# Kernel tuning notes

Measured on AMD Instinct MI355X. Metric: run time of the kernel, lower is better.

The kernel has to match this reference:

```python
import jax, jax.numpy as jnp
import numpy as np

H = 4      # num_heads
DH = 32    # head dim (hidden_size // num_heads)


def _seg_softmax(logits, seg, n):
    # numerically stable segment softmax over axis 0, segments of size n
    m = jax.ops.segment_max(logits, seg, num_segments=n)
    e = jnp.exp(logits - m[seg])
    s = jax.ops.segment_sum(e, seg, num_segments=n)
    return e / (s[seg] + 1e-16)


def setup_inputs() -> dict:
    key = jax.random.key(0)
    ks = jax.random.split(key, 16)
    N, E, EE, C = 50000, 400000, 800000, 800000
    NIN, EIN, HID, EMB = 1, 32, 128, 32
    inp = {
        'x': jax.random.normal(ks[0], (N, NIN), jnp.float32),
        'edge_index': jax.random.randint(ks[1], (2, E), 0, N),
        'edge_attr': jax.random.normal(ks[2], (E, EIN), jnp.float32),
        'edge_to_edge_index': jax.random.randint(ks[3], (2, EE), 0, E),
        'node_to_node_index': jax.random.randint(ks[4], (2, C), 0, N),
        'W1': jax.random.normal(ks[5], (2 * NIN + EIN, EMB), jnp.float32) / np.sqrt(2 * NIN + EIN),
        'b1': jnp.zeros((EMB,), jnp.float32),
        'W2': jax.random.normal(ks[6], (EMB, HID), jnp.float32) / np.sqrt(EMB),
        'b2': jnp.zeros((HID,), jnp.float32),
        'Wq': jax.random.normal(ks[7], (HID, HID), jnp.float32) / np.sqrt(HID),
        'Wk': jax.random.normal(ks[8], (HID, HID), jnp.float32) / np.sqrt(HID),
        'Wv': jax.random.normal(ks[9], (HID, HID), jnp.float32) / np.sqrt(HID),
        'Wq2': jax.random.normal(ks[10], (1, HID), jnp.float32),
        'Wk2': jax.random.normal(ks[11], (1, HID), jnp.float32),
        'Wv2': jax.random.normal(ks[12], (1, HID), jnp.float32),
    }
    return inp


def reference(x, edge_index, edge_attr, edge_to_edge_index, node_to_node_index,
              W1, b1, W2, b2, Wq, Wk, Wv, Wq2, Wk2, Wv2):
    N = x.shape[0]
    E = edge_attr.shape[0]
    # --- NodeToEdgeAggregation: gather endpoint node feats, concat edge attr, MLP ---
    s, d = edge_index[0], edge_index[1]
    h = jnp.concatenate([x[s], x[d], edge_attr], axis=-1)          # [E, 2*nin+ein]
    h = jax.nn.relu(h @ W1 + b1) @ W2 + b2                          # [E, hidden]
    # --- EdgeToEdgeAggregation: multi-head attention on the line graph ---
    es, ed = edge_to_edge_index[0], edge_to_edge_index[1]
    q = (h @ Wq)[ed].reshape(-1, H, DH)                             # [EE, H, DH]
    k = (h @ Wk)[es].reshape(-1, H, DH)
    v = (h @ Wv)[es].reshape(-1, H, DH)
    logits = (q * k).sum(-1) / jnp.sqrt(jnp.float32(DH))            # [EE, H]
    alpha = _seg_softmax(logits, ed, E)                             # softmax over incoming edge-neighbors
    agg_e = jax.ops.segment_sum(alpha[..., None] * v, ed, num_segments=E)  # [E, H, DH]
    updated_edge_feat = agg_e.reshape(E, -1).mean(axis=1, keepdims=True)   # [E, 1]
    # --- EdgeToNodeAggregation over combined node+edge feature array ---
    nef = jnp.concatenate([x, updated_edge_feat], axis=0)           # [N+E, 1]
    ns, nd = node_to_node_index[0], node_to_node_index[1]
    q2 = (nef[nd] @ Wq2).reshape(-1, H, DH)                         # [C, H, DH]
    k2 = (nef[ns] @ Wk2).reshape(-1, H, DH)
    v2 = (nef[ns] @ Wv2).reshape(-1, H, DH)
    logits2 = (q2 * k2).sum(-1) / jnp.sqrt(jnp.float32(DH))         # [C, H]
    alpha2 = _seg_softmax(logits2, nd, N + E)
    msgs = (alpha2[..., None] * v2).reshape(ns.shape[0], -1).mean(axis=1)  # [C]
    aggregated_node_feat = jax.ops.segment_sum(msgs, nd, num_segments=N)   # [N]
    return (aggregated_node_feat, updated_edge_feat)
```

## Files before the change

kernel.cpp:

```cpp
#include <hip/hip_runtime.h>
#include <stdint.h>

#define HIDN 128
#define EMBN 32
#define PCAP 16
#define NCAP 64
#define PSEGSH 10
#define NSEGSH 7
#define PSEG (1 << PSEGSH)
#define NSEG (1 << NSEGSH)
#define PBCAP 2816
#define NBCAP 2816
#define CHUNK 2048
#define MAXBINS 400

typedef __attribute__((ext_vector_type(8))) short bf16x8;
typedef __attribute__((ext_vector_type(4))) float f32x4;
typedef unsigned long long u64;

__device__ __forceinline__ unsigned bf16r(float f) {
  unsigned u = __float_as_uint(f);
  return (u + 0x7FFFu + ((u >> 16) & 1u)) >> 16;
}
__device__ __forceinline__ unsigned pack2(float a, float b) {
  return bf16r(a) | (bf16r(b) << 16);
}
__device__ __forceinline__ float blo(unsigned u) { return __uint_as_float(u << 16); }
__device__ __forceinline__ float bhi(unsigned u) { return __uint_as_float(u & 0xFFFF0000u); }
__device__ __forceinline__ float4 f4fma(float s, float4 a, float4 b) {
  return make_float4(fmaf(s, a.x, b.x), fmaf(s, a.y, b.y), fmaf(s, a.z, b.z), fmaf(s, a.w, b.w));
}
__device__ __forceinline__ float4 f4max0(float4 a) {
  return make_float4(fmaxf(a.x, 0.f), fmaxf(a.y, 0.f), fmaxf(a.z, 0.f), fmaxf(a.w, 0.f));
}

__global__ __launch_bounds__(256) void k_prep1(
    const float* __restrict__ W2, const float* __restrict__ b2,
    const float* __restrict__ Wq, const float* __restrict__ Wk, const float* __restrict__ Wv,
    float* __restrict__ Wqp, float* __restrict__ Wkp, float* __restrict__ bqp,
    float* __restrict__ Wvsp, float* __restrict__ bvs)
{
  __shared__ float swvs[HIDN * 4];
  int t = threadIdx.x;
  if (blockIdx.x == 33) {
    for (int idx = t; idx < HIDN * 4; idx += 256) {
      int l = idx >> 2, h = idx & 3;
      float s = 0.f;
      const float* wl = Wv + l * HIDN + h * 32;
      for (int dh = 0; dh < 32; dh++) s += wl[dh];
      swvs[idx] = s;
    }
    __syncthreads();
    if (t < 128) {
      int i = t >> 2, h = t & 3;
      float a = 0.f;
      for (int l = 0; l < HIDN; l++) a = fmaf(W2[i * HIDN + l], swvs[l * 4 + h], a);
      Wvsp[t] = a;
    } else if (t < 132) {
      int h = t - 128;
      float a = 0.f;
      for (int l = 0; l < HIDN; l++) a = fmaf(b2[l], swvs[l * 4 + h], a);
      bvs[h] = a;
    }
    return;
  }
  int idx = blockIdx.x * 256 + t;
  if (idx < 8192) {
    int q = idx < 4096;
    int tt = q ? idx : idx - 4096;
    int i = tt >> 7, j = tt & 127;
    const float* W = q ? Wq : Wk;
    float a = 0.f;
    for (int l = 0; l < HIDN; l++)
      a = fmaf(W2[i * HIDN + l], W[l * HIDN + j], a);
    (q ? Wqp : Wkp)[tt] = a;
  } else if (idx < 8320) {
    int j = idx - 8192;
    float a = 0.f;
    for (int l = 0; l < HIDN; l++)
      a = fmaf(b2[l], Wq[l * HIDN + j], a);
    bqp[j] = a;
  }
}

__global__ __launch_bounds__(256, 4) void k_front(
    const float* __restrict__ x, const int* __restrict__ eidx, const float* __restrict__ ea,
    const float* __restrict__ W1, const float* __restrict__ b1,
    const float* __restrict__ Wvsp, const float* __restrict__ bvs,
    unsigned* __restrict__ embB, uint2* __restrict__ vsb,
    const int* __restrict__ e2e, int* __restrict__ goffP, u64* __restrict__ partP,
    const int* __restrict__ n2n, int* __restrict__ goffN, u64* __restrict__ partN,
    int E, int EE, int C, int N, int nEdgeB, int nPartP, int PBINS, int NBINS)
{
  __shared__ int lcnt[MAXBINS];
  __shared__ int lbase[MAXBINS];
  int b = blockIdx.x;
  int tid = threadIdx.x;
  if (b < nEdgeB) {
    int e = b * 256 + tid;
    if (e >= E) return;
    int si = eidx[e], di = eidx[E + e];
    float xs = x[si], xd = x[di];

    const float4* b4  = (const float4*)b1;
    const float4* w0  = (const float4*)W1;
    const float4* w1r = (const float4*)(W1 + 32);
    float4 E0, E1, E2, E3, E4, E5, E6, E7;
#define INIT(i) E##i = f4fma(xs, w0[i], f4fma(xd, w1r[i], b4[i]));
    INIT(0) INIT(1) INIT(2) INIT(3) INIT(4) INIT(5) INIT(6) INIT(7)
#undef INIT
    const float4* ea4 = (const float4*)(ea + (size_t)e * 32);
#define ROW(c, wr) { const float4* w_ = (const float4*)(W1 + (size_t)(wr) * 32); \
  E0 = f4fma(c, w_[0], E0); E1 = f4fma(c, w_[1], E1); E2 = f4fma(c, w_[2], E2); E3 = f4fma(c, w_[3], E3); \
  E4 = f4fma(c, w_[4], E4); E5 = f4fma(c, w_[5], E5); E6 = f4fma(c, w_[6], E6); E7 = f4fma(c, w_[7], E7); }
#pragma unroll
    for (int rb = 0; rb < 8; rb++) {
      float4 v = ea4[rb];
      ROW(v.x, 2 + rb * 4 + 0)
      ROW(v.y, 2 + rb * 4 + 1)
      ROW(v.z, 2 + rb * 4 + 2)
      ROW(v.w, 2 + rb * 4 + 3)
    }
#undef ROW
    E0 = f4max0(E0); E1 = f4max0(E1); E2 = f4max0(E2); E3 = f4max0(E3);
    E4 = f4max0(E4); E5 = f4max0(E5); E6 = f4max0(E6); E7 = f4max0(E7);

    uint4 p0, p1, p2, p3;
    p0.x = pack2(E0.x, E0.y); p0.y = pack2(E0.z, E0.w); p0.z = pack2(E1.x, E1.y); p0.w = pack2(E1.z, E1.w);
    p1.x = pack2(E2.x, E2.y); p1.y = pack2(E2.z, E2.w); p1.z = pack2(E3.x, E3.y); p1.w = pack2(E3.z, E3.w);
    p2.x = pack2(E4.x, E4.y); p2.y = pack2(E4.z, E4.w); p2.z = pack2(E5.x, E5.y); p2.w = pack2(E5.z, E5.w);
    p3.x = pack2(E6.x, E6.y); p3.y = pack2(E6.z, E6.w); p3.z = pack2(E7.x, E7.y); p3.w = pack2(E7.z, E7.w);
    uint4* er = (uint4*)(embB + (size_t)e * 16);
    er[0] = p0; er[1] = p1; er[2] = p2; er[3] = p3;

    const float4* wv = (const float4*)Wvsp;
    float4 vs = *(const float4*)bvs;
#define VK(k) { vs = f4fma(E##k.x, wv[4*k+0], vs); vs = f4fma(E##k.y, wv[4*k+1], vs); \
                vs = f4fma(E##k.z, wv[4*k+2], vs); vs = f4fma(E##k.w, wv[4*k+3], vs); }
    VK(0) VK(1) VK(2) VK(3) VK(4) VK(5) VK(6) VK(7)
#undef VK
    vsb[e] = make_uint2(pack2(vs.x, vs.y), pack2(vs.z, vs.w));
  } else if (b < nEdgeB + nPartP) {
    int start = (b - nEdgeB) * CHUNK;
    for (int i = tid; i < PBINS; i += 256) lcnt[i] = 0;
    __syncthreads();
#pragma unroll 4
    for (int k = 0; k < 8; k++) {
      int p = start + k * 256 + tid;
      if (p < EE) atomicAdd(&lcnt[e2e[EE + p] >> PSEGSH], 1);
    }
    __syncthreads();
    for (int i = tid; i < PBINS; i += 256) {
      int c = lcnt[i];
      lbase[i] = c ? atomicAdd(&goffP[i], c) : 0;
      lcnt[i] = 0;
    }
    __syncthreads();
#pragma unroll 4
    for (int k = 0; k < 8; k++) {
      int p = start + k * 256 + tid;
      if (p < EE) {
        int es = e2e[p], ed = e2e[EE + p];
        int bin = ed >> PSEGSH;
        int pos = atomicAdd(&lcnt[bin], 1) + lbase[bin];
        if (pos < PBCAP)
          partP[(size_t)bin * PBCAP + pos] = ((u64)(unsigned)ed << 32) | (unsigned)es;
      }
    }
  } else {
    int start = (b - nEdgeB - nPartP) * CHUNK;
    for (int i = tid; i < NBINS; i += 256) lcnt[i] = 0;
    __syncthreads();
#pragma unroll 4
    for (int k = 0; k < 8; k++) {
      int c = start + k * 256 + tid;
      if (c < C) {
        int nd = n2n[C + c];
        if (nd < N) atomicAdd(&lcnt[nd >> NSEGSH], 1);
      }
    }
    __syncthreads();
    for (int i = tid; i < NBINS; i += 256) {
      int c = lcnt[i];
      lbase[i] = c ? atomicAdd(&goffN[i], c) : 0;
      lcnt[i] = 0;
    }
    __syncthreads();
#pragma unroll 4
    for (int k = 0; k < 8; k++) {
      int c = start + k * 256 + tid;
      if (c < C) {
        int ns = n2n[c], nd = n2n[C + c];
        if (nd < N) {
          int bin = nd >> NSEGSH;
          unsigned pay = __float_as_uint(x[ns]);
          int pos = atomicAdd(&lcnt[bin], 1) + lbase[bin];
          if (pos < NBCAP)
            partN[(size_t)bin * NBCAP + pos] = ((u64)(unsigned)nd << 32) | pay;
        }
      }
    }
  }
}

__global__ __launch_bounds__(256) void k_fill(
    const int* __restrict__ goffP, const u64* __restrict__ partP,
    int* __restrict__ pcnt, int* __restrict__ pbucket,
    const float* __restrict__ Wqp, const float* __restrict__ Wkp,
    const float* __restrict__ bqp,
    const float* __restrict__ Wq2, const float* __restrict__ Wk2, const float* __restrict__ Wv2,
    unsigned short* __restrict__ MBpk, float* __restrict__ c2th,
    float* __restrict__ dhd, float* __restrict__ wv2s,
    int E, int PBINS)
{
  extern __shared__ int lds[];
  const float rs = 0.17677669529663687f;
  int b = blockIdx.x;
  int tid = threadIdx.x;
  if (b < PBINS) {
    int seg0 = b << PSEGSH;
    int nseg = E - seg0; if (nseg > PSEG) nseg = PSEG;
    int* cnt = lds;
    int* rows = lds + PSEG;
    for (int i = tid; i < nseg; i += 256) cnt[i] = 0;
    __syncthreads();
    int g = goffP[b]; if (g > PBCAP) g = PBCAP;
    for (int i = tid; i < g; i += 256) {
      u64 pk = partP[(size_t)b * PBCAP + i];
      int ed = (int)(pk >> 32);
      int es = (int)(unsigned)pk;
      int s = ed - seg0;
      int pos = atomicAdd(&cnt[s], 1);
      if (pos < PCAP) rows[s * PCAP + pos] = es;
    }
    __syncthreads();
    for (int i = tid; i < nseg; i += 256) pcnt[seg0 + i] = cnt[i];
    int tot = nseg * PCAP;
    for (int i = tid; i < tot; i += 256)
      pbucket[(size_t)seg0 * PCAP + i] = rows[i];
  } else {
    int idx = (b - PBINS) * 256 + tid;
    if (idx < 4096) {
      int jj = idx & 7, lane = (idx >> 3) & 63, nb = (idx >> 9) & 1, h = idx >> 10;
      int k = (lane >> 4) * 8 + jj;
      int n = nb * 16 + (lane & 15);
      float a = 0.f;
      const float* wq = Wqp + k * HIDN + h * 32;
      const float* wk = Wkp + n * HIDN + h * 32;
      for (int j = 0; j < 32; j++) a = fmaf(wq[j], wk[j], a);
      MBpk[idx] = (unsigned short)bf16r(a * rs);
    } else if (idx < 4224) {
      int t = idx - 4096;
      int h = t >> 5, ip = t & 31;
      float a2 = 0.f;
      for (int j = 0; j < 32; j++)
        a2 = fmaf(bqp[h * 32 + j], Wkp[ip * HIDN + h * 32 + j], a2);
      c2th[h * 32 + ip] = a2 * rs;
    } else if (idx < 4228) {
      int h = idx - 4224;
      float d = 0.f, wsum = 0.f;
      for (int dh = 0; dh < 32; dh++) {
        d = fmaf(Wq2[h * 32 + dh], Wk2[h * 32 + dh], d);
        wsum += Wv2[h * 32 + dh];
      }
      dhd[h]  = d * rs;
      wv2s[h] = wsum;
    }
  }
}

__global__ __launch_bounds__(256, 4) void k_back(
    const unsigned* __restrict__ embB, const unsigned short* __restrict__ MBpk,
    const uint2* __restrict__ vsb, const float* __restrict__ c2th,
    const int* __restrict__ pcnt, const int* __restrict__ pbucket,
    const int* __restrict__ goffN, const u64* __restrict__ partN,
    const float* __restrict__ x, const float* __restrict__ dhd, const float* __restrict__ wv2s,
    float* __restrict__ out0, float* __restrict__ out1,
    int E, int N, int NBINS)
{
  __shared__ float qtl[256 * 33];
  int b = blockIdx.x;
  int tid = threadIdx.x;
  if (b < NBINS) {
    int seg0 = b << NSEGSH;
    int nseg = N - seg0; if (nseg > NSEG) nseg = NSEG;
    int* cnt = (int*)qtl;
    float* rows = qtl + NSEG;
    for (int i = tid; i < nseg; i += 256) cnt[i] = 0;
    __syncthreads();
    int g = goffN[b]; if (g > NBCAP) g = NBCAP;
    for (int i = tid; i < g; i += 256) {
      u64 pk = partN[(size_t)b * NBCAP + i];
      int nd = (int)(pk >> 32);
      int s = nd - seg0;
      int pos = atomicAdd(&cnt[s], 1);
      if (pos < NCAP) rows[s * NCAP + pos] = __uint_as_float((unsigned)pk);
    }
    __syncthreads();
    for (int t = tid; t < nseg * 4; t += 256) {
      int s = t >> 2, h = t & 3;
      int c = cnt[s]; c = c < NCAP ? c : NCAP;
      int nd = seg0 + s;
      float xn = x[nd];
      float d = dhd[h];
      const float* bkt = rows + s * NCAP;

      float amx = -3.4e38f, amn = 3.4e38f;
      for (int n = 0; n < c; n++) {
        float a = xn * bkt[n];
        amx = fmaxf(amx, a); amn = fminf(amn, a);
      }
      float m = (d > 0.f) ? d * amx : d * amn;

      float den = 0.f, num = 0.f;
      for (int n = 0; n < c; n++) {
        float asv = bkt[n];
        float ev = __expf(fmaf(xn * asv, d, -m));
        den += ev;
        num = fmaf(ev, asv, num);
      }
      float r = wv2s[h] * num / (den + 1e-16f);
      r += __shfl_xor(r, 1);
      r += __shfl_xor(r, 2);
      if (h == 0) out0[nd] = r * 0.0078125f;
    }
  } else {
    int pb = b - NBINS;
    int wave = tid >> 6, lane = tid & 63;
    int e0 = pb * 64;
    int we0 = e0 + wave * 16;

    union { uint4 u; bf16x8 bv; } af;
    af.u = *((const uint4*)(embB + ((size_t)(we0 + (lane & 15)) << 4)) + (lane >> 4));

#pragma unroll
    for (int h = 0; h < 4; h++) {
#pragma unroll
      for (int nb = 0; nb < 2; nb++) {
        union { uint4 u; bf16x8 bv; } bf;
        bf.u = *(const uint4*)(MBpk + (((h * 2 + nb) * 64 + lane) << 3));
        int col = nb * 16 + (lane & 15);
        float c2v = c2th[h * 32 + col];
        f32x4 acc = {c2v, c2v, c2v, c2v};
        acc = __builtin_amdgcn_mfma_f32_16x16x32_bf16(af.bv, bf.bv, acc, 0, 0, 0);
        int rowb = wave * 16 + (lane >> 4) * 4;
#pragma unroll
        for (int r = 0; r < 4; r++)
          qtl[((rowb + r) * 4 + h) * 33 + col] = acc[r];
      }
    }
    __syncthreads();

    int e = e0 + (tid >> 2);
    if (e >= E) return;
    int h = tid & 3;
    const float* q = qtl + tid * 33;

    int cnt = pcnt[e];
    cnt = cnt < PCAP ? cnt : PCAP;
    float den = 0.f, num = 0.f;
    for (int n = 0; n < cnt; n++) {
      int es = pbucket[(size_t)e * PCAP + n];
      const uint4* ep = (const uint4*)(embB + ((size_t)es << 4));
      uint4 u0 = ep[0], u1 = ep[1], u2 = ep[2], u3 = ep[3];
      uint2 vu = vsb[es];
      unsigned vh = (h & 2) ? vu.y : vu.x;
      float vsv = (h & 1) ? bhi(vh) : blo(vh);
      float dot = 0.f;
#define DOT8(uu, base) \
      dot = fmaf(q[base + 0], blo(uu.x), dot); dot = fmaf(q[base + 1], bhi(uu.x), dot); \
      dot = fmaf(q[base + 2], blo(uu.y), dot); dot = fmaf(q[base + 3], bhi(uu.y), dot); \
      dot = fmaf(q[base + 4], blo(uu.z), dot); dot = fmaf(q[base + 5], bhi(uu.z), dot); \
      dot = fmaf(q[base + 6], blo(uu.w), dot); dot = fmaf(q[base + 7], bhi(uu.w), dot);
      DOT8(u0, 0) DOT8(u1, 8) DOT8(u2, 16) DOT8(u3, 24)
#undef DOT8
      float ex = __expf(dot);
      den += ex;
      num = fmaf(ex, vsv, num);
    }
    float r = num / (den + 1e-16f);
    r += __shfl_xor(r, 1);
    r += __shfl_xor(r, 2);
    if (h == 0) out1[e] = r * 0.0078125f;
  }
}

extern "C" void kernel_launch(void* const* d_in, const int* in_sizes, int n_in,
                              void* d_out, int out_size, void* d_ws, size_t ws_size,
                              hipStream_t stream)
{
  const float* x   = (const float*)d_in[0];
  const int*   eidx= (const int*)d_in[1];
  const float* ea  = (const float*)d_in[2];
  const int*   e2e = (const int*)d_in[3];
  const int*   n2n = (const int*)d_in[4];
  const float* W1  = (const float*)d_in[5];
  const float* b1  = (const float*)d_in[6];
  const float* W2  = (const float*)d_in[7];
  const float* b2  = (const float*)d_in[8];
  const float* Wq  = (const float*)d_in[9];
  const float* Wk  = (const float*)d_in[10];
  const float* Wv  = (const float*)d_in[11];
  const float* Wq2 = (const float*)d_in[12];
  const float* Wk2 = (const float*)d_in[13];
  const float* Wv2 = (const float*)d_in[14];

  const int N  = in_sizes[0];
  const int E  = in_sizes[1] / 2;
  const int EE = in_sizes[3] / 2;
  const int C  = in_sizes[4] / 2;

  float* out0 = (float*)d_out;
  float* out1 = (float*)d_out + N;

  const int PBINS = (E + PSEG - 1) >> PSEGSH;
  const int NBINS = (N + NSEG - 1) >> NSEGSH;

  char* w = (char*)d_ws;
  size_t off = 0;
  auto alloc = [&](size_t bytes) -> char* {
    char* p = w + off;
    off += (bytes + 255) & ~(size_t)255;
    return p;
  };
  float* Wqp   = (float*)alloc(EMBN * HIDN * 4);
  float* Wkp   = (float*)alloc(EMBN * HIDN * 4);
  float* bqp   = (float*)alloc(HIDN * 4);
  unsigned short* MBpk = (unsigned short*)alloc(4096 * 2);
  float* c2th  = (float*)alloc(4 * EMBN * 4);
  float* Wvsp  = (float*)alloc(EMBN * 4 * 4);
  float* bvs   = (float*)alloc(16);
  float* dhd   = (float*)alloc(16);
  float* wv2s  = (float*)alloc(16);
  unsigned* embB = (unsigned*)alloc((size_t)E * 16 * 4);
  uint2* vsb   = (uint2*)alloc((size_t)E * 8);
  u64*   partP = (u64*)alloc((size_t)PBINS * PBCAP * 8);
  u64*   partN = (u64*)alloc((size_t)NBINS * NBCAP * 8);
  int*   pbucket = (int*)alloc((size_t)E * PCAP * 4);
  int*   pcnt  = (int*)alloc((size_t)E * 4);
  char* zbase = w + off;
  int*   goffP = (int*)alloc((size_t)PBINS * 4);
  int*   goffN = (int*)alloc((size_t)NBINS * 4);
  size_t zbytes = (size_t)((w + off) - zbase);

  const int nEdgeB = (E + 255) / 256;
  const int nPartP = (EE + CHUNK - 1) / CHUNK;
  const int nPartN = (C + CHUNK - 1) / CHUNK;
  const int nPairMfmaB = (E + 63) / 64;
  const int nPrep2B = 17;
  const size_t fillLDS = (size_t)(PSEG + PSEG * PCAP) * 4;

  hipMemsetAsync(zbase, 0, zbytes, stream);

  k_prep1<<<34, 256, 0, stream>>>(W2, b2, Wq, Wk, Wv, Wqp, Wkp, bqp, Wvsp, bvs);
  k_front<<<nEdgeB + nPartP + nPartN, 256, 0, stream>>>(
      x, eidx, ea, W1, b1, Wvsp, bvs, embB, vsb,
      e2e, goffP, partP, n2n, goffN, partN,
      E, EE, C, N, nEdgeB, nPartP, PBINS, NBINS);
  k_fill<<<PBINS + nPrep2B, 256, fillLDS, stream>>>(
      goffP, partP, pcnt, pbucket,
      Wqp, Wkp, bqp, Wq2, Wk2, Wv2, MBpk, c2th, dhd, wv2s, E, PBINS);
  k_back<<<NBINS + nPairMfmaB, 256, 0, stream>>>(
      embB, MBpk, vsb, c2th, pcnt, pbucket, goffN, partN,
      x, dhd, wv2s, out0, out1, E, N, NBINS);
}
```

Before: 235.7 us.

## Replace two-pass binned partition with direct global-atomic bucket fill

The LDS-staged binning pass (per-chunk histogram, global offset reservation, partition into bins) followed by a separate k_fill kernel is replaced by direct global atomicAdd on per-destination counters that write straight into fixed-capacity buckets. The weight-prep work from k_fill moves into k_front as extra blocks, removing one kernel launch. The node-side back kernel now loads its buckets from a dense per-node array into padded LDS rows. The cost is many scattered global atomics and uncoalesced writes in place of local LDS atomics, plus a larger memset over the per-node counters and ordering that is no longer deterministic.

```diff
diff --git a/kernel.cpp b/kernel.cpp
--- a/kernel.cpp
+++ b/kernel.cpp
@@ -5,14 +5,9 @@
 #define EMBN 32
 #define PCAP 16
 #define NCAP 64
-#define PSEGSH 10
 #define NSEGSH 7
-#define PSEG (1 << PSEGSH)
 #define NSEG (1 << NSEGSH)
-#define PBCAP 2816
-#define NBCAP 2816
 #define CHUNK 2048
-#define MAXBINS 400
 
 typedef __attribute__((ext_vector_type(8))) short bf16x8;
 typedef __attribute__((ext_vector_type(4))) float f32x4;
@@ -88,12 +83,14 @@
     const float* __restrict__ W1, const float* __restrict__ b1,
     const float* __restrict__ Wvsp, const float* __restrict__ bvs,
     unsigned* __restrict__ embB, uint2* __restrict__ vsb,
-    const int* __restrict__ e2e, int* __restrict__ goffP, u64* __restrict__ partP,
-    const int* __restrict__ n2n, int* __restrict__ goffN, u64* __restrict__ partN,
-    int E, int EE, int C, int N, int nEdgeB, int nPartP, int PBINS, int NBINS)
+    const int* __restrict__ e2e, int* __restrict__ pcnt, int* __restrict__ pbucket,
+    const int* __restrict__ n2n, int* __restrict__ ncnt, float* __restrict__ nbucket,
+    const float* __restrict__ Wqp, const float* __restrict__ Wkp, const float* __restrict__ bqp,
+    const float* __restrict__ Wq2, const float* __restrict__ Wk2, const float* __restrict__ Wv2,
+    unsigned short* __restrict__ MBpk, float* __restrict__ c2th,
+    float* __restrict__ dhd, float* __restrict__ wv2s,
+    int E, int EE, int C, int N, int nEdgeB, int nPartP, int nPartN)
 {
-  __shared__ int lcnt[MAXBINS];
-  __shared__ int lbase[MAXBINS];
   int b = blockIdx.x;
   int tid = threadIdx.x;
   if (b < nEdgeB) {
@@ -142,104 +139,31 @@
     vsb[e] = make_uint2(pack2(vs.x, vs.y), pack2(vs.z, vs.w));
   } else if (b < nEdgeB + nPartP) {
     int start = (b - nEdgeB) * CHUNK;
-    for (int i = tid; i < PBINS; i += 256) lcnt[i] = 0;
-    __syncthreads();
-#pragma unroll 4
-    for (int k = 0; k < 8; k++) {
-      int p = start + k * 256 + tid;
-      if (p < EE) atomicAdd(&lcnt[e2e[EE + p] >> PSEGSH], 1);
-    }
-    __syncthreads();
-    for (int i = tid; i < PBINS; i += 256) {
-      int c = lcnt[i];
-      lbase[i] = c ? atomicAdd(&goffP[i], c) : 0;
-      lcnt[i] = 0;
-    }
-    __syncthreads();
 #pragma unroll 4
     for (int k = 0; k < 8; k++) {
       int p = start + k * 256 + tid;
       if (p < EE) {
         int es = e2e[p], ed = e2e[EE + p];
-        int bin = ed >> PSEGSH;
-        int pos = atomicAdd(&lcnt[bin], 1) + lbase[bin];
-        if (pos < PBCAP)
-          partP[(size_t)bin * PBCAP + pos] = ((u64)(unsigned)ed << 32) | (unsigned)es;
-      }
-    }
-  } else {
+        int pos = atomicAdd(&pcnt[ed], 1);
+        if (pos < PCAP) pbucket[(size_t)ed * PCAP + pos] = es;
+      }
+    }
+  } else if (b < nEdgeB + nPartP + nPartN) {
     int start = (b - nEdgeB - nPartP) * CHUNK;
-    for (int i = tid; i < NBINS; i += 256) lcnt[i] = 0;
-    __syncthreads();
-#pragma unroll 4
-    for (int k = 0; k < 8; k++) {
-      int c = start + k * 256 + tid;
-      if (c < C) {
-        int nd = n2n[C + c];
-        if (nd < N) atomicAdd(&lcnt[nd >> NSEGSH], 1);
-      }
-    }
-    __syncthreads();
-    for (int i = tid; i < NBINS; i += 256) {
-      int c = lcnt[i];
-      lbase[i] = c ? atomicAdd(&goffN[i], c) : 0;
-      lcnt[i] = 0;
-    }
-    __syncthreads();
 #pragma unroll 4
     for (int k = 0; k < 8; k++) {
       int c = start + k * 256 + tid;
       if (c < C) {
         int ns = n2n[c], nd = n2n[C + c];
         if (nd < N) {
-          int bin = nd >> NSEGSH;
-          unsigned pay = __float_as_uint(x[ns]);
-          int pos = atomicAdd(&lcnt[bin], 1) + lbase[bin];
-          if (pos < NBCAP)
-            partN[(size_t)bin * NBCAP + pos] = ((u64)(unsigned)nd << 32) | pay;
+          int pos = atomicAdd(&ncnt[nd], 1);
+          if (pos < NCAP) nbucket[((size_t)nd << 6) + pos] = x[ns];
         }
       }
     }
-  }
-}
-
-__global__ __launch_bounds__(256) void k_fill(
-    const int* __restrict__ goffP, const u64* __restrict__ partP,
-    int* __restrict__ pcnt, int* __restrict__ pbucket,
-    const float* __restrict__ Wqp, const float* __restrict__ Wkp,
-    const float* __restrict__ bqp,
-    const float* __restrict__ Wq2, const float* __restrict__ Wk2, const float* __restrict__ Wv2,
-    unsigned short* __restrict__ MBpk, float* __restrict__ c2th,
-    float* __restrict__ dhd, float* __restrict__ wv2s,
-    int E, int PBINS)
-{
-  extern __shared__ int lds[];
-  const float rs = 0.17677669529663687f;
-  int b = blockIdx.x;
-  int tid = threadIdx.x;
-  if (b < PBINS) {
-    int seg0 = b << PSEGSH;
-    int nseg = E - seg0; if (nseg > PSEG) nseg = PSEG;
-    int* cnt = lds;
-    int* rows = lds + PSEG;
-    for (int i = tid; i < nseg; i += 256) cnt[i] = 0;
-    __syncthreads();
-    int g = goffP[b]; if (g > PBCAP) g = PBCAP;
-    for (int i = tid; i < g; i += 256) {
-      u64 pk = partP[(size_t)b * PBCAP + i];
-      int ed = (int)(pk >> 32);
-      int es = (int)(unsigned)pk;
-      int s = ed - seg0;
-      int pos = atomicAdd(&cnt[s], 1);
-      if (pos < PCAP) rows[s * PCAP + pos] = es;
-    }
-    __syncthreads();
-    for (int i = tid; i < nseg; i += 256) pcnt[seg0 + i] = cnt[i];
-    int tot = nseg * PCAP;
-    for (int i = tid; i < tot; i += 256)
-      pbucket[(size_t)seg0 * PCAP + i] = rows[i];
   } else {
-    int idx = (b - PBINS) * 256 + tid;
+    const float rs = 0.17677669529663687f;
+    int idx = (b - nEdgeB - nPartP - nPartN) * 256 + tid;
     if (idx < 4096) {
       int jj = idx & 7, lane = (idx >> 3) & 63, nb = (idx >> 9) & 1, h = idx >> 10;
       int k = (lane >> 4) * 8 + jj;
@@ -273,7 +197,7 @@
     const unsigned* __restrict__ embB, const unsigned short* __restrict__ MBpk,
     const uint2* __restrict__ vsb, const float* __restrict__ c2th,
     const int* __restrict__ pcnt, const int* __restrict__ pbucket,
-    const int* __restrict__ goffN, const u64* __restrict__ partN,
+    const int* __restrict__ ncnt, const float* __restrict__ nbucket,
     const float* __restrict__ x, const float* __restrict__ dhd, const float* __restrict__ wv2s,
     float* __restrict__ out0, float* __restrict__ out1,
     int E, int N, int NBINS)
@@ -286,24 +210,23 @@
     int nseg = N - seg0; if (nseg > NSEG) nseg = NSEG;
     int* cnt = (int*)qtl;
     float* rows = qtl + NSEG;
-    for (int i = tid; i < nseg; i += 256) cnt[i] = 0;
+    for (int i = tid; i < nseg; i += 256) {
+      int c = ncnt[seg0 + i];
+      cnt[i] = c < NCAP ? c : NCAP;
+    }
     __syncthreads();
-    int g = goffN[b]; if (g > NBCAP) g = NBCAP;
-    for (int i = tid; i < g; i += 256) {
-      u64 pk = partN[(size_t)b * NBCAP + i];
-      int nd = (int)(pk >> 32);
-      int s = nd - seg0;
-      int pos = atomicAdd(&cnt[s], 1);
-      if (pos < NCAP) rows[s * NCAP + pos] = __uint_as_float((unsigned)pk);
+    for (int idx = tid; idx < nseg * NCAP; idx += 256) {
+      int s = idx >> 6, n = idx & 63;
+      if (n < cnt[s]) rows[s * (NCAP + 1) + n] = nbucket[((size_t)(seg0 + s) << 6) + n];
     }
     __syncthreads();
     for (int t = tid; t < nseg * 4; t += 256) {
       int s = t >> 2, h = t & 3;
-      int c = cnt[s]; c = c < NCAP ? c : NCAP;
+      int c = cnt[s];
       int nd = seg0 + s;
       float xn = x[nd];
       float d = dhd[h];
-      const float* bkt = rows + s * NCAP;
+      const float* bkt = rows + s * (NCAP + 1);
 
       float amx = -3.4e38f, amn = 3.4e38f;
       for (int n = 0; n < c; n++) {
@@ -413,7 +336,6 @@
   float* out0 = (float*)d_out;
   float* out1 = (float*)d_out + N;
 
-  const int PBINS = (E + PSEG - 1) >> PSEGSH;
   const int NBINS = (N + NSEG - 1) >> NSEGSH;
 
   char* w = (char*)d_ws;
@@ -434,13 +356,11 @@
   float* wv2s  = (float*)alloc(16);
   unsigned* embB = (unsigned*)alloc((size_t)E * 16 * 4);
   uint2* vsb   = (uint2*)alloc((size_t)E * 8);
-  u64*   partP = (u64*)alloc((size_t)PBINS * PBCAP * 8);
-  u64*   partN = (u64*)alloc((size_t)NBINS * NBCAP * 8);
   int*   pbucket = (int*)alloc((size_t)E * PCAP * 4);
+  float* nbucket = (float*)alloc((size_t)N * NCAP * 4);
+  char* zbase = w + off;
   int*   pcnt  = (int*)alloc((size_t)E * 4);
-  char* zbase = w + off;
-  int*   goffP = (int*)alloc((size_t)PBINS * 4);
-  int*   goffN = (int*)alloc((size_t)NBINS * 4);
+  int*   ncnt  = (int*)alloc((size_t)N * 4);
   size_t zbytes = (size_t)((w + off) - zbase);
 
   const int nEdgeB = (E + 255) / 256;
@@ -448,19 +368,16 @@
   const int nPartN = (C + CHUNK - 1) / CHUNK;
   const int nPairMfmaB = (E + 63) / 64;
   const int nPrep2B = 17;
-  const size_t fillLDS = (size_t)(PSEG + PSEG * PCAP) * 4;
 
   hipMemsetAsync(zbase, 0, zbytes, stream);
 
   k_prep1<<<34, 256, 0, stream>>>(W2, b2, Wq, Wk, Wv, Wqp, Wkp, bqp, Wvsp, bvs);
-  k_front<<<nEdgeB + nPartP + nPartN, 256, 0, stream>>>(
+  k_front<<<nEdgeB + nPartP + nPartN + nPrep2B, 256, 0, stream>>>(
       x, eidx, ea, W1, b1, Wvsp, bvs, embB, vsb,
-      e2e, goffP, partP, n2n, goffN, partN,
-      E, EE, C, N, nEdgeB, nPartP, PBINS, NBINS);
-  k_fill<<<PBINS + nPrep2B, 256, fillLDS, stream>>>(
-      goffP, partP, pcnt, pbucket,
-      Wqp, Wkp, bqp, Wq2, Wk2, Wv2, MBpk, c2th, dhd, wv2s, E, PBINS);
+      e2e, pcnt, pbucket, n2n, ncnt, nbucket,
+      Wqp, Wkp, bqp, Wq2, Wk2, Wv2, MBpk, c2th, dhd, wv2s,
+      E, EE, C, N, nEdgeB, nPartP, nPartN);
   k_back<<<NBINS + nPairMfmaB, 256, 0, stream>>>(
-      embB, MBpk, vsb, c2th, pcnt, pbucket, goffN, partN,
+      embB, MBpk, vsb, c2th, pcnt, pbucket, ncnt, nbucket,
       x, dhd, wv2s, out0, out1, E, N, NBINS);
 }
```

After: 293.9 us. 24.7% more time.

## Prefetch first four neighbor gathers, move prep2 into front kernel, pad LDS rows

Applied to the files above, without the earlier changes.

The edge-attention loop in k_back now loads the first four bucket indices as one uint4 and issues all four embedding and value gathers before any dot products. This is meant to overlap memory latency across neighbors instead of serializing each gather. The weight-precompute blocks (MBpk, c2th, dhd, wv2s) move from k_fill into extra blocks of k_front, which shortens k_fill's critical path. Node bucket rows in LDS are padded to NCAP+1 to reduce bank conflicts. The unrolled gathers cost more registers, and the loads for slots past cnt still fetch row 0.

```diff
diff --git a/kernel.cpp b/kernel.cpp
--- a/kernel.cpp
+++ b/kernel.cpp
@@ -90,7 +90,11 @@
     unsigned* __restrict__ embB, uint2* __restrict__ vsb,
     const int* __restrict__ e2e, int* __restrict__ goffP, u64* __restrict__ partP,
     const int* __restrict__ n2n, int* __restrict__ goffN, u64* __restrict__ partN,
-    int E, int EE, int C, int N, int nEdgeB, int nPartP, int PBINS, int NBINS)
+    const float* __restrict__ Wqp, const float* __restrict__ Wkp, const float* __restrict__ bqp,
+    const float* __restrict__ Wq2, const float* __restrict__ Wk2, const float* __restrict__ Wv2,
+    unsigned short* __restrict__ MBpk, float* __restrict__ c2th,
+    float* __restrict__ dhd, float* __restrict__ wv2s,
+    int E, int EE, int C, int N, int nEdgeB, int nPartP, int nPartN, int PBINS, int NBINS)
 {
   __shared__ int lcnt[MAXBINS];
   __shared__ int lbase[MAXBINS];
@@ -167,7 +171,7 @@
           partP[(size_t)bin * PBCAP + pos] = ((u64)(unsigned)ed << 32) | (unsigned)es;
       }
     }
-  } else {
+  } else if (b < nEdgeB + nPartP + nPartN) {
     int start = (b - nEdgeB - nPartP) * CHUNK;
     for (int i = tid; i < NBINS; i += 256) lcnt[i] = 0;
     __syncthreads();
@@ -200,46 +204,9 @@
         }
       }
     }
-  }
-}
-
-__global__ __launch_bounds__(256) void k_fill(
-    const int* __restrict__ goffP, const u64* __restrict__ partP,
-    int* __restrict__ pcnt, int* __restrict__ pbucket,
-    const float* __restrict__ Wqp, const float* __restrict__ Wkp,
-    const float* __restrict__ bqp,
-    const float* __restrict__ Wq2, const float* __restrict__ Wk2, const float* __restrict__ Wv2,
-    unsigned short* __restrict__ MBpk, float* __restrict__ c2th,
-    float* __restrict__ dhd, float* __restrict__ wv2s,
-    int E, int PBINS)
-{
-  extern __shared__ int lds[];
-  const float rs = 0.17677669529663687f;
-  int b = blockIdx.x;
-  int tid = threadIdx.x;
-  if (b < PBINS) {
-    int seg0 = b << PSEGSH;
-    int nseg = E - seg0; if (nseg > PSEG) nseg = PSEG;
-    int* cnt = lds;
-    int* rows = lds + PSEG;
-    for (int i = tid; i < nseg; i += 256) cnt[i] = 0;
-    __syncthreads();
-    int g = goffP[b]; if (g > PBCAP) g = PBCAP;
-    for (int i = tid; i < g; i += 256) {
-      u64 pk = partP[(size_t)b * PBCAP + i];
-      int ed = (int)(pk >> 32);
-      int es = (int)(unsigned)pk;
-      int s = ed - seg0;
-      int pos = atomicAdd(&cnt[s], 1);
-      if (pos < PCAP) rows[s * PCAP + pos] = es;
-    }
-    __syncthreads();
-    for (int i = tid; i < nseg; i += 256) pcnt[seg0 + i] = cnt[i];
-    int tot = nseg * PCAP;
-    for (int i = tid; i < tot; i += 256)
-      pbucket[(size_t)seg0 * PCAP + i] = rows[i];
   } else {
-    int idx = (b - PBINS) * 256 + tid;
+    const float rs = 0.17677669529663687f;
+    int idx = (b - nEdgeB - nPartP - nPartN) * 256 + tid;
     if (idx < 4096) {
       int jj = idx & 7, lane = (idx >> 3) & 63, nb = (idx >> 9) & 1, h = idx >> 10;
       int k = (lane >> 4) * 8 + jj;
@@ -269,6 +236,36 @@
   }
 }
 
+__global__ __launch_bounds__(256) void k_fill(
+    const int* __restrict__ goffP, const u64* __restrict__ partP,
+    int* __restrict__ pcnt, int* __restrict__ pbucket,
+    int E)
+{
+  extern __shared__ int lds[];
+  int b = blockIdx.x;
+  int tid = threadIdx.x;
+  int seg0 = b << PSEGSH;
+  int nseg = E - seg0; if (nseg > PSEG) nseg = PSEG;
+  int* cnt = lds;
+  int* rows = lds + PSEG;
+  for (int i = tid; i < nseg; i += 256) cnt[i] = 0;
+  __syncthreads();
+  int g = goffP[b]; if (g > PBCAP) g = PBCAP;
+  for (int i = tid; i < g; i += 256) {
+    u64 pk = partP[(size_t)b * PBCAP + i];
+    int ed = (int)(pk >> 32);
+    int es = (int)(unsigned)pk;
+    int s = ed - seg0;
+    int pos = atomicAdd(&cnt[s], 1);
+    if (pos < PCAP) rows[s * PCAP + pos] = es;
+  }
+  __syncthreads();
+  for (int i = tid; i < nseg; i += 256) pcnt[seg0 + i] = cnt[i];
+  int tot = nseg * PCAP;
+  for (int i = tid; i < tot; i += 256)
+    pbucket[(size_t)seg0 * PCAP + i] = rows[i];
+}
+
 __global__ __launch_bounds__(256, 4) void k_back(
     const unsigned* __restrict__ embB, const unsigned short* __restrict__ MBpk,
     const uint2* __restrict__ vsb, const float* __restrict__ c2th,
@@ -294,7 +291,7 @@
       int nd = (int)(pk >> 32);
       int s = nd - seg0;
       int pos = atomicAdd(&cnt[s], 1);
-      if (pos < NCAP) rows[s * NCAP + pos] = __uint_as_float((unsigned)pk);
+      if (pos < NCAP) rows[s * (NCAP + 1) + pos] = __uint_as_float((unsigned)pk);
     }
     __syncthreads();
     for (int t = tid; t < nseg * 4; t += 256) {
@@ -303,7 +300,7 @@
       int nd = seg0 + s;
       float xn = x[nd];
       float d = dhd[h];
-      const float* bkt = rows + s * NCAP;
+      const float* bkt = rows + s * (NCAP + 1);
 
       float amx = -3.4e38f, amn = 3.4e38f;
       for (int n = 0; n < c; n++) {
@@ -358,26 +355,52 @@
 
     int cnt = pcnt[e];
     cnt = cnt < PCAP ? cnt : PCAP;
+
+    uint4 r0 = *(const uint4*)(pbucket + ((size_t)e << 4));
+    int s0 = (cnt > 0) ? r0.x : 0;
+    int s1 = (cnt > 1) ? r0.y : 0;
+    int s2 = (cnt > 2) ? r0.z : 0;
+    int s3 = (cnt > 3) ? r0.w : 0;
+
+#define GATH(i) \
+    const uint4* ep##i = (const uint4*)(embB + ((size_t)s##i << 4)); \
+    uint4 u##i##0 = ep##i[0], u##i##1 = ep##i[1], u##i##2 = ep##i[2], u##i##3 = ep##i[3]; \
+    uint2 vu##i = vsb[s##i];
+    GATH(0) GATH(1) GATH(2) GATH(3)
+#undef GATH
+
     float den = 0.f, num = 0.f;
-    for (int n = 0; n < cnt; n++) {
-      int es = pbucket[(size_t)e * PCAP + n];
-      const uint4* ep = (const uint4*)(embB + ((size_t)es << 4));
-      uint4 u0 = ep[0], u1 = ep[1], u2 = ep[2], u3 = ep[3];
-      uint2 vu = vsb[es];
-      unsigned vh = (h & 2) ? vu.y : vu.x;
-      float vsv = (h & 1) ? bhi(vh) : blo(vh);
-      float dot = 0.f;
 #define DOT8(uu, base) \
       dot = fmaf(q[base + 0], blo(uu.x), dot); dot = fmaf(q[base + 1], bhi(uu.x), dot); \
       dot = fmaf(q[base + 2], blo(uu.y), dot); dot = fmaf(q[base + 3], bhi(uu.y), dot); \
       dot = fmaf(q[base + 4], blo(uu.z), dot); dot = fmaf(q[base + 5], bhi(uu.z), dot); \
       dot = fmaf(q[base + 6], blo(uu.w), dot); dot = fmaf(q[base + 7], bhi(uu.w), dot);
-      DOT8(u0, 0) DOT8(u1, 8) DOT8(u2, 16) DOT8(u3, 24)
-#undef DOT8
+#define SLOT(i) { \
+      float dot = 0.f; \
+      DOT8(u##i##0, 0) DOT8(u##i##1, 8) DOT8(u##i##2, 16) DOT8(u##i##3, 24) \
+      unsigned vh = (h & 2) ? vu##i.y : vu##i.x; \
+      float vsv = (h & 1) ? bhi(vh) : blo(vh); \
+      float ex = (i < cnt) ? __expf(dot) : 0.f; \
+      den += ex; \
+      num = fmaf(ex, vsv, num); }
+    SLOT(0) SLOT(1) SLOT(2) SLOT(3)
+#undef SLOT
+
+    for (int n = 4; n < cnt; n++) {
+      int es = pbucket[((size_t)e << 4) + n];
+      const uint4* ep = (const uint4*)(embB + ((size_t)es << 4));
+      uint4 t0 = ep[0], t1 = ep[1], t2 = ep[2], t3 = ep[3];
+      uint2 vu = vsb[es];
+      unsigned vh = (h & 2) ? vu.y : vu.x;
+      float vsv = (h & 1) ? bhi(vh) : blo(vh);
+      float dot = 0.f;
+      DOT8(t0, 0) DOT8(t1, 8) DOT8(t2, 16) DOT8(t3, 24)
       float ex = __expf(dot);
       den += ex;
       num = fmaf(ex, vsv, num);
     }
+#undef DOT8
+
     float r = num / (den + 1e-16f);
     r += __shfl_xor(r, 1);
     r += __shfl_xor(r, 2);
@@ -453,13 +476,12 @@
   hipMemsetAsync(zbase, 0, zbytes, stream);
 
   k_prep1<<<34, 256, 0, stream>>>(W2, b2, Wq, Wk, Wv, Wqp, Wkp, bqp, Wvsp, bvs);
-  k_front<<<nEdgeB + nPartP + nPartN, 256, 0, stream>>>(
+  k_front<<<nEdgeB + nPartP + nPartN + nPrep2B, 256, 0, stream>>>(
       x, eidx, ea, W1, b1, Wvsp, bvs, embB, vsb,
       e2e, goffP, partP, n2n, goffN, partN,
-      E, EE, C, N, nEdgeB, nPartP, PBINS, NBINS);
-  k_fill<<<PBINS + nPrep2B, 256, fillLDS, stream>>>(
-      goffP, partP, pcnt, pbucket,
-      Wqp, Wkp, bqp, Wq2, Wk2, Wv2, MBpk, c2th, dhd, wv2s, E, PBINS);
+      Wqp, Wkp, bqp, Wq2, Wk2, Wv2, MBpk, c2th, dhd, wv2s,
+      E, EE, C, N, nEdgeB, nPartP, nPartN, PBINS, NBINS);
+  k_fill<<<PBINS, 256, fillLDS, stream>>>(goffP, partP, pcnt, pbucket, E);
   k_back<<<NBINS + nPairMfmaB, 256, 0, stream>>>(
       embB, MBpk, vsb, c2th, pcnt, pbucket, goffN, partN,
       x, dhd, wv2s, out0, out1, E, N, NBINS);
```

Result: slower. 241.6 us (+2.5%).
